# Optimization experiments

Measured on AMD Instinct MI355X. Metric: run time of the kernel, lower is better.

The kernel has to match this reference:

```python
import jax, jax.numpy as jnp
import numpy as np

D_MODEL = 1024
NUM_HEADS = 16
D_K = D_MODEL // NUM_HEADS


def setup_inputs() -> dict:
    key = jax.random.key(0)
    k1, k2, k3, k4 = jax.random.split(key, 4)
    scale = 1.0 / np.sqrt(D_MODEL)
    inp = {
        "input": jax.random.normal(k1, (2, 2048, D_MODEL), dtype=jnp.float32),
        "W_qkv": jax.random.normal(k2, (D_MODEL, 3 * D_MODEL), dtype=jnp.float32) * scale,
        "b_qkv": jax.random.normal(k3, (3 * D_MODEL,), dtype=jnp.float32) * 0.02,
        "W_out": jax.random.normal(k4, (D_MODEL, D_MODEL), dtype=jnp.float32) * scale,
    }
    return inp


def reference(input, W_qkv, b_qkv, W_out):
    B, S, _ = input.shape
    qkv = input @ W_qkv + b_qkv                      # [B,S,3D]
    q, k, v = jnp.split(qkv, 3, axis=-1)             # each [B,S,D]
    def heads(x):
        return x.reshape(B, S, NUM_HEADS, D_K).transpose(0, 2, 1, 3)  # [B,H,S,dk]
    q, k, v = heads(q), heads(k), heads(v)
    scores = jnp.einsum("bhsd,bhtd->bhst", q, k) / jnp.sqrt(jnp.float32(D_K))
    attn = jax.nn.softmax(scores, axis=-1)           # [B,H,S,S]
    out = jnp.einsum("bhst,bhtd->bhsd", attn, v)     # [B,H,S,dk]
    out = out.transpose(0, 2, 1, 3).reshape(B, S, D_MODEL)
    return out @ W_out
```

## Files before the change

### kernel.cpp

```cpp
#include <hip/hip_runtime.h>

typedef unsigned short u16;
typedef unsigned int u32;
typedef __attribute__((ext_vector_type(8))) short short8;
typedef __attribute__((ext_vector_type(8))) __bf16 bf16x8;
typedef __attribute__((ext_vector_type(4))) float f32x4;

__device__ __forceinline__ u16 f2bf(float f) {
  union { float f; u32 u; } c; c.f = f;
  u32 u = c.u + 0x7fffu + ((c.u >> 16) & 1u);
  return (u16)(u >> 16);
}
__device__ __forceinline__ f32x4 mfma16(short8 a, short8 b, f32x4 c) {
  return __builtin_amdgcn_mfma_f32_16x16x32_bf16(
      __builtin_bit_cast(bf16x8, a), __builtin_bit_cast(bf16x8, b), c, 0, 0, 0);
}

__global__ __launch_bounds__(256) void transpose_f32_bf16(const float* __restrict__ in,
                                                          u16* __restrict__ out,
                                                          int R, int C) {
  __shared__ u16 tile[32][33];
  int tx = threadIdx.x & 31, ty = threadIdx.x >> 5;
  int c0 = blockIdx.x * 32, r0 = blockIdx.y * 32;
  for (int i = 0; i < 32; i += 8)
    tile[ty + i][tx] = f2bf(in[(size_t)(r0 + ty + i) * C + c0 + tx]);
  __syncthreads();
  for (int i = 0; i < 32; i += 8)
    out[(size_t)(c0 + ty + i) * R + r0 + tx] = tile[tx][ty + i];
}

template <bool HAS_BIAS, bool AF32, bool OUTF32, bool ROUTE>
__global__ __launch_bounds__(256) void gemm_bt(const void* __restrict__ Av,
                                               const u16* __restrict__ BT,
                                               const float* __restrict__ bias,
                                               void* __restrict__ C0v,
                                               void* __restrict__ C1v,
                                               int M, int N, int K) {
  __shared__ __align__(16) u16 As[128 * 72];
  __shared__ __align__(16) u16 Bs[128 * 72];
  const int tid = threadIdx.x;
  const int w = tid >> 6, l = tid & 63;
  const int i16 = l & 15, q4 = l >> 4;
  const int m0 = blockIdx.y * 128, n0 = blockIdx.x * 128;
  const int wm = (w >> 1) * 64, wn = (w & 1) * 64;

  f32x4 acc[4][4] = {};

  for (int k0 = 0; k0 < K; k0 += 64) {
    __syncthreads();
    for (int i = 0; i < 4; ++i) {
      int idx = i * 256 + tid;
      int row = idx >> 3, kg = (idx & 7) * 8;
      if (AF32) {
        const float* src = (const float*)Av + (size_t)(m0 + row) * K + k0 + kg;
        float4 f0 = *(const float4*)src;
        float4 f1 = *(const float4*)(src + 4);
        short8 v;
        v[0] = (short)f2bf(f0.x); v[1] = (short)f2bf(f0.y);
        v[2] = (short)f2bf(f0.z); v[3] = (short)f2bf(f0.w);
        v[4] = (short)f2bf(f1.x); v[5] = (short)f2bf(f1.y);
        v[6] = (short)f2bf(f1.z); v[7] = (short)f2bf(f1.w);
        *(short8*)&As[row * 72 + kg] = v;
      } else {
        *(short8*)&As[row * 72 + kg] =
            *(const short8*)((const u16*)Av + (size_t)(m0 + row) * K + k0 + kg);
      }
      *(short8*)&Bs[row * 72 + kg] =
          *(const short8*)&BT[(size_t)(n0 + row) * K + k0 + kg];
    }
    __syncthreads();
    for (int ks = 0; ks < 2; ++ks) {
      short8 af[4], bfr[4];
      for (int mi = 0; mi < 4; ++mi)
        af[mi] = *(short8*)&As[(wm + mi * 16 + i16) * 72 + ks * 32 + q4 * 8];
      for (int ni = 0; ni < 4; ++ni)
        bfr[ni] = *(short8*)&Bs[(wn + ni * 16 + i16) * 72 + ks * 32 + q4 * 8];
      for (int mi = 0; mi < 4; ++mi)
        for (int ni = 0; ni < 4; ++ni)
          acc[mi][ni] = mfma16(af[mi], bfr[ni], acc[mi][ni]);
    }
  }

  u16* dstb; float* dstf = nullptr; int ldc, cb;
  if (ROUTE) {
    if (n0 < 1024) { dstb = (u16*)C0v; ldc = 1024; cb = n0; }
    else           { dstb = (u16*)C1v; ldc = 2048; cb = n0 - 1024; }
  } else {
    if (OUTF32) dstf = (float*)C0v; else dstb = (u16*)C0v;
    ldc = N; cb = n0;
  }

  for (int mi = 0; mi < 4; ++mi) {
    int row = m0 + wm + mi * 16 + q4 * 4;
    for (int ni = 0; ni < 4; ++ni) {
      int nl = wn + ni * 16 + i16;
      float b = HAS_BIAS ? bias[n0 + nl] : 0.0f;
      for (int r = 0; r < 4; ++r) {
        float v = acc[mi][ni][r] + b;
        if (!ROUTE && OUTF32)
          dstf[(size_t)(row + r) * ldc + cb + nl] = v;
        else
          dstb[(size_t)(row + r) * ldc + cb + nl] = f2bf(v);
      }
    }
  }
}

__global__ __launch_bounds__(512) void attn_flash(u16* __restrict__ Qbuf,
                                                  const u16* __restrict__ KVall) {
  constexpr float CSC = 0.18033688011112042f;
  constexpr float MC  = 96.0f * CSC;
  __shared__ __align__(16) u16 Qs[128 * 72];
  __shared__ __align__(16) u16 Ks[64 * 72];
  __shared__ __align__(16) u16 Vt[64 * 72];
  __shared__ __align__(16) u16 Ps[8 * 16 * 72];

  const int tid = threadIdx.x;
  const int w = tid >> 6, l = tid & 63;
  const int i16 = l & 15, q4 = l >> 4;
  const int h = blockIdx.y;
  const int q0 = blockIdx.x * 128;
  u16* Q = Qbuf + (size_t)blockIdx.z * 2048 * 1024;
  const u16* KV = KVall + (size_t)blockIdx.z * 2048 * 2048;

  for (int i = 0; i < 2; ++i) {
    int idx = i * 512 + tid;
    int row = idx >> 3, col = (idx & 7) * 8;
    *(short8*)&Qs[row * 72 + col] =
        *(const short8*)&Q[(size_t)(q0 + row) * 1024 + h * 64 + col];
  }
  __syncthreads();

  short8 qf[2];
  for (int ks = 0; ks < 2; ++ks)
    qf[ks] = *(short8*)&Qs[(w * 16 + i16) * 72 + ks * 32 + q4 * 8];

  short8 ones;
#pragma unroll
  for (int j = 0; j < 8; ++j) ones[j] = (short)0x3F80;

  f32x4 o[4] = {};
  f32x4 lacc = {};

  for (int t0 = 0; t0 < 2048; t0 += 64) {
    __syncthreads();
    {
      int row = tid >> 3, sc = tid & 7, col = sc * 8;
      *(short8*)&Ks[row * 72 + col] =
          *(const short8*)&KV[(size_t)(t0 + row) * 2048 + h * 64 + col];
      short8 rv = *(const short8*)&KV[(size_t)(t0 + row) * 2048 + 1024 + h * 64 + col];
#pragma unroll
      for (int jj = 0; jj < 8; ++jj) {
        int j = (jj + sc) & 7;
        Vt[(col + j) * 72 + row] = (u16)rv[j];
      }
    }
    __syncthreads();

    f32x4 s[4] = {};
    for (int ks = 0; ks < 2; ++ks)
      for (int nt = 0; nt < 4; ++nt) {
        short8 kf = *(short8*)&Ks[(nt * 16 + i16) * 72 + ks * 32 + q4 * 8];
        s[nt] = mfma16(qf[ks], kf, s[nt]);
      }

#pragma unroll
    for (int r = 0; r < 4; ++r)
#pragma unroll
      for (int nt = 0; nt < 4; ++nt) {
        float p = exp2f(__builtin_fmaf(s[nt][r], CSC, -MC));
        Ps[w * 1152 + (q4 * 4 + r) * 72 + nt * 16 + i16] =
            (u16)(__builtin_bit_cast(u32, p) >> 16);
      }
    __syncthreads();

    for (int ks2 = 0; ks2 < 2; ++ks2) {
      short8 pf = *(short8*)&Ps[w * 1152 + i16 * 72 + ks2 * 32 + q4 * 8];
      lacc = mfma16(pf, ones, lacc);
      for (int nd = 0; nd < 4; ++nd) {
        short8 vf = *(short8*)&Vt[(nd * 16 + i16) * 72 + ks2 * 32 + q4 * 8];
        o[nd] = mfma16(pf, vf, o[nd]);
      }
    }
  }

  for (int r = 0; r < 4; ++r) {
    float inv = 1.0f / lacc[r];
    int row = q0 + w * 16 + q4 * 4 + r;
    for (int nd = 0; nd < 4; ++nd)
      Q[(size_t)row * 1024 + h * 64 + nd * 16 + i16] = f2bf(o[nd][r] * inv);
  }
}

extern "C" void kernel_launch(void* const* d_in, const int* in_sizes, int n_in,
                              void* d_out, int out_size, void* d_ws, size_t ws_size,
                              hipStream_t stream) {
  const float* X    = (const float*)d_in[0];
  const float* Wqkv = (const float*)d_in[1];
  const float* bqkv = (const float*)d_in[2];
  const float* Wout = (const float*)d_in[3];

  u16* Qbuf = (u16*)d_out;
  u16* WT1  = Qbuf + (size_t)4096 * 1024;
  u16* WT2  = WT1 + (size_t)3072 * 1024;
  u16* KV   = (u16*)d_ws;
  float* Cws = (float*)d_ws;

  transpose_f32_bf16<<<dim3(96, 32), 256, 0, stream>>>(Wqkv, WT1, 1024, 3072);
  transpose_f32_bf16<<<dim3(32, 32), 256, 0, stream>>>(Wout, WT2, 1024, 1024);

  gemm_bt<true, true, false, true><<<dim3(24, 32), 256, 0, stream>>>(
      X, WT1, bqkv, Qbuf, KV, 4096, 3072, 1024);

  attn_flash<<<dim3(16, 16, 2), 512, 0, stream>>>(Qbuf, KV);

  gemm_bt<false, false, true, false><<<dim3(8, 32), 256, 0, stream>>>(
      Qbuf, WT2, nullptr, Cws, nullptr, 4096, 1024, 1024);

  hipMemcpyAsync(d_out, Cws, (size_t)4096 * 1024 * sizeof(float),
                 hipMemcpyDeviceToDevice, stream);
}
```

Baseline: 254.5 us.

## Rewrite attention with 32x32 MFMA, register-resident P and permlane swaps

The attention kernel moves from 16x16x32 to 32x32x16 bf16 MFMA with 4 waves of 32 query rows each. Scores are computed transposed (K as the A operand), so the exponentiated probabilities can be packed with v_cvt_pk_bf16_f32 and rearranged with v_permlane32_swap instead of going through an LDS round trip and an extra barrier. Row sums are accumulated in scalar registers rather than with an extra MFMA against a ones vector. Q is loaded straight from global memory into registers. Block size halves to 256 threads, which lowers per-block parallelism and raises register pressure per wave.

```diff
diff --git a/kernel.cpp b/kernel.cpp
--- a/kernel.cpp
+++ b/kernel.cpp
@@ -5,6 +5,7 @@
 typedef __attribute__((ext_vector_type(8))) short short8;
 typedef __attribute__((ext_vector_type(8))) __bf16 bf16x8;
 typedef __attribute__((ext_vector_type(4))) float f32x4;
+typedef __attribute__((ext_vector_type(16))) float f32x16;
 
 __device__ __forceinline__ u16 f2bf(float f) {
   union { float f; u32 u; } c; c.f = f;
@@ -13,6 +14,10 @@
 }
 __device__ __forceinline__ f32x4 mfma16(short8 a, short8 b, f32x4 c) {
   return __builtin_amdgcn_mfma_f32_16x16x32_bf16(
+      __builtin_bit_cast(bf16x8, a), __builtin_bit_cast(bf16x8, b), c, 0, 0, 0);
+}
+__device__ __forceinline__ f32x16 mfma32(short8 a, short8 b, f32x16 c) {
+  return __builtin_amdgcn_mfma_f32_32x32x16_bf16(
       __builtin_bit_cast(bf16x8, a), __builtin_bit_cast(bf16x8, b), c, 0, 0, 0);
 }
 
@@ -106,89 +111,106 @@
   }
 }
 
-__global__ __launch_bounds__(512) void attn_flash(u16* __restrict__ Qbuf,
+__global__ __launch_bounds__(256) void attn_flash(u16* __restrict__ Qbuf,
                                                   const u16* __restrict__ KVall) {
   constexpr float CSC = 0.18033688011112042f;
   constexpr float MC  = 96.0f * CSC;
-  __shared__ __align__(16) u16 Qs[128 * 72];
   __shared__ __align__(16) u16 Ks[64 * 72];
   __shared__ __align__(16) u16 Vt[64 * 72];
-  __shared__ __align__(16) u16 Ps[8 * 16 * 72];
+  __shared__ float Rs[4 * 32];
 
   const int tid = threadIdx.x;
   const int w = tid >> 6, l = tid & 63;
-  const int i16 = l & 15, q4 = l >> 4;
+  const int l31 = l & 31, hi = l >> 5;
   const int h = blockIdx.y;
   const int q0 = blockIdx.x * 128;
   u16* Q = Qbuf + (size_t)blockIdx.z * 2048 * 1024;
   const u16* KV = KVall + (size_t)blockIdx.z * 2048 * 2048;
 
-  for (int i = 0; i < 2; ++i) {
-    int idx = i * 512 + tid;
-    int row = idx >> 3, col = (idx & 7) * 8;
-    *(short8*)&Qs[row * 72 + col] =
-        *(const short8*)&Q[(size_t)(q0 + row) * 1024 + h * 64 + col];
-  }
+  short8 qf[4];
+  {
+    const u16* qrow = Q + (size_t)(q0 + w * 32 + l31) * 1024 + h * 64 + hi * 8;
+#pragma unroll
+    for (int ks = 0; ks < 4; ++ks) qf[ks] = *(const short8*)(qrow + ks * 16);
+  }
+
+  f32x16 o0 = {}, o1 = {};
+  float sm0 = 0.f, sm1 = 0.f, sm2 = 0.f, sm3 = 0.f;
+
+  const int srow = tid >> 3, sc = tid & 7, scol = sc * 8;
+
+  for (int t0 = 0; t0 < 2048; t0 += 64) {
+    __syncthreads();
+#pragma unroll
+    for (int rr = 0; rr < 2; ++rr) {
+      const int row = srow + rr * 32;
+      *(short8*)&Ks[row * 72 + scol] =
+          *(const short8*)&KV[(size_t)(t0 + row) * 2048 + h * 64 + scol];
+      short8 rv = *(const short8*)&KV[(size_t)(t0 + row) * 2048 + 1024 + h * 64 + scol];
+#pragma unroll
+      for (int jj = 0; jj < 8; ++jj) {
+        const int j = (jj + sc) & 7;
+        Vt[(scol + j) * 72 + row] = (u16)rv[j];
+      }
+    }
+    __syncthreads();
+
+    f32x16 st0 = {}, st1 = {};
+#pragma unroll
+    for (int ks = 0; ks < 4; ++ks) {
+      short8 kf0 = *(short8*)&Ks[l31 * 72 + ks * 16 + hi * 8];
+      short8 kf1 = *(short8*)&Ks[(32 + l31) * 72 + ks * 16 + hi * 8];
+      st0 = mfma32(kf0, qf[ks], st0);
+      st1 = mfma32(kf1, qf[ks], st1);
+    }
+
+    u32 W[16];
+#define SOFTMAX_PACK(stt, WB)                                               \
+    {                                                                       \
+      float p_[16];                                                         \
+      _Pragma("unroll") for (int r = 0; r < 16; ++r)                        \
+          p_[r] = exp2f(__builtin_fmaf(stt[r], CSC, -MC));                  \
+      _Pragma("unroll") for (int r = 0; r < 16; r += 4) {                   \
+        sm0 += p_[r]; sm1 += p_[r + 1]; sm2 += p_[r + 2]; sm3 += p_[r + 3]; \
+      }                                                                     \
+      _Pragma("unroll") for (int m = 0; m < 4; ++m)                         \
+        _Pragma("unroll") for (int s = 0; s < 2; ++s)                       \
+          asm("v_cvt_pk_bf16_f32 %0, %1, %2"                                \
+              : "=v"(W[(WB) + m * 2 + s])                                   \
+              : "v"(p_[4 * m + 2 * s]), "v"(p_[4 * m + 2 * s + 1]));        \
+    }
+    SOFTMAX_PACK(st0, 0)
+    SOFTMAX_PACK(st1, 8)
+#undef SOFTMAX_PACK
+
+#pragma unroll
+    for (int u = 0; u < 4; ++u) {
+      const int base = (u >> 1) * 8 + (u & 1) * 4;
+      u32 a0 = W[base], a1 = W[base + 1], b0 = W[base + 2], b1 = W[base + 3];
+      asm("v_permlane32_swap_b32 %0, %1" : "+v"(a0), "+v"(b0));
+      asm("v_permlane32_swap_b32 %0, %1" : "+v"(a1), "+v"(b1));
+      int4 af4;
+      af4.x = (int)a0; af4.y = (int)a1; af4.z = (int)b0; af4.w = (int)b1;
+      const short8 pf = __builtin_bit_cast(short8, af4);
+      const short8 vf0 = *(short8*)&Vt[l31 * 72 + u * 16 + hi * 8];
+      const short8 vf1 = *(short8*)&Vt[(32 + l31) * 72 + u * 16 + hi * 8];
+      o0 = mfma32(pf, vf0, o0);
+      o1 = mfma32(pf, vf1, o1);
+    }
+  }
+
+  float rs = (sm0 + sm1) + (sm2 + sm3);
+  rs += __shfl_xor(rs, 32);
+  if (hi == 0) Rs[w * 32 + l31] = rs;
   __syncthreads();
 
-  short8 qf[2];
-  for (int ks = 0; ks < 2; ++ks)
-    qf[ks] = *(short8*)&Qs[(w * 16 + i16) * 72 + ks * 32 + q4 * 8];
-
-  short8 ones;
-#pragma unroll
-  for (int j = 0; j < 8; ++j) ones[j] = (short)0x3F80;
-
-  f32x4 o[4] = {};
-  f32x4 lacc = {};
-
-  for (int t0 = 0; t0 < 2048; t0 += 64) {
-    __syncthreads();
-    {
-      int row = tid >> 3, sc = tid & 7, col = sc * 8;
-      *(short8*)&Ks[row * 72 + col] =
-          *(const short8*)&KV[(size_t)(t0 + row) * 2048 + h * 64 + col];
-      short8 rv = *(const short8*)&KV[(size_t)(t0 + row) * 2048 + 1024 + h * 64 + col];
-#pragma unroll
-      for (int jj = 0; jj < 8; ++jj) {
-        int j = (jj + sc) & 7;
-        Vt[(col + j) * 72 + row] = (u16)rv[j];
-      }
-    }
-    __syncthreads();
-
-    f32x4 s[4] = {};
-    for (int ks = 0; ks < 2; ++ks)
-      for (int nt = 0; nt < 4; ++nt) {
-        short8 kf = *(short8*)&Ks[(nt * 16 + i16) * 72 + ks * 32 + q4 * 8];
-        s[nt] = mfma16(qf[ks], kf, s[nt]);
-      }
-
-#pragma unroll
-    for (int r = 0; r < 4; ++r)
-#pragma unroll
-      for (int nt = 0; nt < 4; ++nt) {
-        float p = exp2f(__builtin_fmaf(s[nt][r], CSC, -MC));
-        Ps[w * 1152 + (q4 * 4 + r) * 72 + nt * 16 + i16] =
-            (u16)(__builtin_bit_cast(u32, p) >> 16);
-      }
-    __syncthreads();
-
-    for (int ks2 = 0; ks2 < 2; ++ks2) {
-      short8 pf = *(short8*)&Ps[w * 1152 + i16 * 72 + ks2 * 32 + q4 * 8];
-      lacc = mfma16(pf, ones, lacc);
-      for (int nd = 0; nd < 4; ++nd) {
-        short8 vf = *(short8*)&Vt[(nd * 16 + i16) * 72 + ks2 * 32 + q4 * 8];
-        o[nd] = mfma16(pf, vf, o[nd]);
-      }
-    }
-  }
-
-  for (int r = 0; r < 4; ++r) {
-    float inv = 1.0f / lacc[r];
-    int row = q0 + w * 16 + q4 * 4 + r;
-    for (int nd = 0; nd < 4; ++nd)
-      Q[(size_t)row * 1024 + h * 64 + nd * 16 + i16] = f2bf(o[nd][r] * inv);
+#pragma unroll
+  for (int r = 0; r < 16; ++r) {
+    const int qq = (r & 3) + 8 * (r >> 2) + 4 * hi;
+    const float inv = 1.0f / Rs[w * 32 + qq];
+    u16* dst = Q + (size_t)(q0 + w * 32 + qq) * 1024 + h * 64 + l31;
+    dst[0]  = f2bf(o0[r] * inv);
+    dst[32] = f2bf(o1[r] * inv);
   }
 }
 
@@ -212,7 +234,7 @@
   gemm_bt<true, true, false, true><<<dim3(24, 32), 256, 0, stream>>>(
       X, WT1, bqkv, Qbuf, KV, 4096, 3072, 1024);
 
-  attn_flash<<<dim3(16, 16, 2), 512, 0, stream>>>(Qbuf, KV);
+  attn_flash<<<dim3(16, 16, 2), 256, 0, stream>>>(Qbuf, KV);
 
   gemm_bt<false, false, true, false><<<dim3(8, 32), 256, 0, stream>>>(
       Qbuf, WT2, nullptr, Cws, nullptr, 4096, 1024, 1024);
```

Result: slower. 272.5 us (+7.0%).
